# Optimization experiments

Hardware: AMD Instinct MI355X
Metric: run time of the kernel (lower is better)

## Reference

```python
import jax, jax.numpy as jnp
import numpy as np

TAU_PLUS = 0.02
TAU_MINUS = 0.02
TAU_X = 0.101
A_TRIPLET = 0.0065
HOMEOSTATIC_RATE = 0.1
DT = 0.001
SPIKE_P = 0.05  # spike probability used to binarize inputs


def setup_inputs() -> dict:
    key = jax.random.key(0)
    k1, k2, k3 = jax.random.split(key, 3)
    B, P, Q, T = 16, 2048, 2048, 256
    pre_spikes = (jax.random.uniform(k1, (B, P, T)) < SPIKE_P).astype(jnp.float32)
    post_spikes = (jax.random.uniform(k2, (B, Q, T)) < SPIKE_P).astype(jnp.float32)
    weights = jax.random.normal(k3, (P, Q), dtype=jnp.float32) * 0.1
    meta_A_plus = jnp.float32(0.01)
    meta_A_minus = jnp.float32(0.012)
    return {"pre_spikes": pre_spikes, "post_spikes": post_spikes,
            "weights": weights, "meta_A_plus": meta_A_plus,
            "meta_A_minus": meta_A_minus}


def _traces(spikes_tbn, decay):
    """Trace value used at step t: x_t = decay * (x_{t-1} + s_{t-1}), x_0 = 0."""
    def step(carry, s):
        x = decay * carry          # decayed trace, used for this step's update
        return x + s, x            # spike added AFTER the update, per original
    init = jnp.zeros(spikes_tbn.shape[1:], spikes_tbn.dtype)
    _, xs = jax.lax.scan(step, init, spikes_tbn)
    return xs  # [T, B, N]


def reference(pre_spikes, post_spikes, weights, meta_A_plus, meta_A_minus):
    B, P, T = pre_spikes.shape
    exp_plus = jnp.exp(jnp.float32(-DT / TAU_PLUS))
    exp_minus = jnp.exp(jnp.float32(-DT / TAU_MINUS))
    exp_x = jnp.exp(jnp.float32(-DT / TAU_X))

    pre_t = jnp.transpose(pre_spikes, (2, 0, 1))    # [T, B, P]
    post_t = jnp.transpose(post_spikes, (2, 0, 1))  # [T, B, Q]

    x_pre = _traces(pre_t, exp_plus)     # [T, B, P]
    x_post = _traces(post_t, exp_minus)  # [T, B, Q]
    x_trip = _traces(post_t, exp_x)      # [T, B, Q]

    # Per-step outer products summed over time == one big contraction over (t, b).
    ltp = jnp.einsum('tbp,tbq->pq', x_pre, post_t) * meta_A_plus
    triplet = jnp.einsum('tbp,tbq->pq', x_pre, post_t * x_trip) * A_TRIPLET
    ltd = jnp.einsum('tbp,tbq->pq', pre_t, x_post) * meta_A_minus
    weight_updates = ltp + triplet - ltd

    # Homeostatic scaling (fresh module: activity history holds only this sample)
    current_activity = (pre_spikes.sum() + post_spikes.sum()) / (B * T)
    scaling_factor = jnp.sqrt(HOMEOSTATIC_RATE / (current_activity + 1e-6))

    updated_weights = weights + weight_updates * scaling_factor
    return jnp.clip(updated_weights, -2.0, 2.0)
```

## Files before the change

kernel.cpp:

```cpp
#include <hip/hip_runtime.h>

constexpr int TB = 16;
constexpr int NP = 2048;
constexpr int NQ = 2048;
constexpr int TT = 256;
constexpr int KH = TB * TT;
constexpr int KT = 2 * KH;

typedef unsigned short ushort_t;
typedef __attribute__((ext_vector_type(8))) __bf16 bf16x8;
typedef __attribute__((ext_vector_type(4))) float f32x4;

__device__ __forceinline__ ushort_t f2bf(float f) {
    unsigned u = __builtin_bit_cast(unsigned, f);
    u = (u + 0x7FFFu + ((u >> 16) & 1u)) >> 16;
    return (ushort_t)u;
}

union Pack16 { ushort_t u[16]; uint4 v[2]; };

constexpr float DF1 = 0.95122942450071400910f;
constexpr float DF2 = DF1 * DF1;
constexpr float DF4 = DF2 * DF2;
constexpr float DF8 = DF4 * DF4;
constexpr float DF16 = DF8 * DF8;
constexpr float DF32 = DF16 * DF16;
constexpr float DF64 = DF32 * DF32;
constexpr float DF128 = DF64 * DF64;

constexpr float DX1 = 0.99014786386058731819f;
constexpr float DX2 = DX1 * DX1;
constexpr float DX4 = DX2 * DX2;
constexpr float DX8 = DX4 * DX4;
constexpr float DX16 = DX8 * DX8;
constexpr float DX32 = DX16 * DX16;
constexpr float DX64 = DX32 * DX32;
constexpr float DX128 = DX64 * DX64;

template <int K>
__device__ __forceinline__ float seg_step(float b, float pw, int sl) {
    float t = __shfl_up(b, K, 64);
    return (sl >= K) ? fmaf(pw, t, b) : b;
}

__global__ __launch_bounds__(256) void stage_traces(
    const float* __restrict__ pre, const float* __restrict__ post,
    const float* __restrict__ mApP, const float* __restrict__ mAmP,
    ushort_t* __restrict__ Ab, ushort_t* __restrict__ Bb,
    float* __restrict__ partials)
{
    const int tid  = threadIdx.x;
    const int lane = tid & 63;
    const int wv   = tid >> 6;
    const int sl   = lane & 15;
    const int seg  = lane >> 4;
    const int rowg = blockIdx.x * 16 + wv * 4 + seg;
    const bool isPre = rowg < TB * NP;
    const int m = isPre ? rowg : rowg - TB * NP;
    const int b = m >> 11;
    const int r = m & 2047;

    const float4* src = (const float4*)((isPre ? pre : post) + (size_t)m * TT);
    float f[16];
    #pragma unroll
    for (int j = 0; j < 4; ++j) {
        float4 u = src[sl * 4 + j];
        f[4 * j] = u.x; f[4 * j + 1] = u.y; f[4 * j + 2] = u.z; f[4 * j + 3] = u.w;
    }
    float cnt = 0.f;
    #pragma unroll
    for (int j = 0; j < 16; ++j) cnt += f[j];

    float Cf = 0.f;
    #pragma unroll
    for (int j = 0; j < 16; ++j) Cf = DF1 * (Cf + f[j]);
    float bs = Cf;
    bs = seg_step<1>(bs, DF16, sl);
    bs = seg_step<2>(bs, DF32, sl);
    bs = seg_step<4>(bs, DF64, sl);
    bs = seg_step<8>(bs, DF128, sl);
    float xinf = __shfl_up(bs, 1, 64);
    if (sl == 0) xinf = 0.f;

    float xf[16];
    {
        float x = xinf;
        #pragma unroll
        for (int j = 0; j < 16; ++j) { xf[j] = x; x = DF1 * (x + f[j]); }
    }

    Pack16 pa, pb;
    if (isPre) {
        #pragma unroll
        for (int j = 0; j < 16; ++j) {
            pa.u[j] = f2bf(xf[j]);
            pb.u[j] = (f[j] != 0.f) ? 0x3F80u : 0u;
        }
    } else {
        float Cx = 0.f;
        #pragma unroll
        for (int j = 0; j < 16; ++j) Cx = DX1 * (Cx + f[j]);
        float bx = Cx;
        bx = seg_step<1>(bx, DX16, sl);
        bx = seg_step<2>(bx, DX32, sl);
        bx = seg_step<4>(bx, DX64, sl);
        bx = seg_step<8>(bx, DX128, sl);
        float xint = __shfl_up(bx, 1, 64);
        if (sl == 0) xint = 0.f;

        const float Ap = *mApP;
        const float Am = *mAmP;
        float xt = xint;
        #pragma unroll
        for (int j = 0; j < 16; ++j) {
            pa.u[j] = (f[j] != 0.f) ? f2bf(fmaf(0.0065f, xt, Ap)) : 0u;
            pb.u[j] = f2bf(-Am * xf[j]);
            xt = DX1 * (xt + f[j]);
        }
    }

    ushort_t* o0 = (isPre ? Ab : Bb) + (size_t)r * KT + b * TT + sl * 16;
    *(uint4*)o0       = pa.v[0];
    *(uint4*)(o0 + 8) = pa.v[1];
    *(uint4*)(o0 + KH)     = pb.v[0];
    *(uint4*)(o0 + KH + 8) = pb.v[1];

    #pragma unroll
    for (int off = 32; off > 0; off >>= 1)
        cnt += __shfl_down(cnt, off, 64);
    __shared__ float wsum[4];
    if (lane == 0) wsum[wv] = cnt;
    __syncthreads();
    if (tid == 0) {
        float s = (wsum[0] + wsum[1]) + (wsum[2] + wsum[3]);
        atomicAdd(&partials[(blockIdx.x & 63) * 16], s);
    }
}

__device__ __forceinline__ void async16(const ushort_t* g, ushort_t* l) {
    __builtin_amdgcn_global_load_lds(
        (const __attribute__((address_space(1))) unsigned int*)g,
        (__attribute__((address_space(3))) unsigned int*)l,
        16, 0, 0);
}

__global__ __launch_bounds__(256) void gemm_split(
    const ushort_t* __restrict__ Ab, const ushort_t* __restrict__ Bb,
    float* __restrict__ P0, float* __restrict__ P1)
{
    __shared__ ushort_t As[2][128 * 64];
    __shared__ ushort_t Bs[2][128 * 64];

    const int tid  = threadIdx.x;
    const int lane = tid & 63;
    const int wv   = tid >> 6;
    const int wr   = wv >> 1;
    const int wc   = wv & 1;
    const int quad = lane >> 4;
    const int m16  = lane & 15;

    const int p0 = blockIdx.y * 128;
    const int q0 = blockIdx.x * 128;
    const int kbase = blockIdx.z * (KT / 2);

    const int ldsbase = wv * 64 * 8;

    f32x4 acc[4][4] = {};

    auto stage = [&](int buf, int k0) {
        #pragma unroll
        for (int rr = 0; rr < 4; ++rr) {
            const int c   = rr * 256 + tid;
            const int row = c >> 3;
            const int kk8 = (c & 7) ^ (row & 7);
            const ushort_t* ga = Ab + (size_t)(p0 + row) * KT + k0 + kk8 * 8;
            const ushort_t* gb = Bb + (size_t)(q0 + row) * KT + k0 + kk8 * 8;
            async16(ga, &As[buf][rr * 256 * 8 + ldsbase]);
            async16(gb, &Bs[buf][rr * 256 * 8 + ldsbase]);
        }
    };

    constexpr int NIT = (KT / 2) / 64;
    stage(0, kbase);

    for (int kt = 0; kt < NIT; ++kt) {
        const int cur = kt & 1;
        __syncthreads();
        if (kt + 1 < NIT)
            stage(cur ^ 1, kbase + (kt + 1) * 64);

        #pragma unroll
        for (int ks = 0; ks < 2; ++ks) {
            bf16x8 af[4], bf[4];
            #pragma unroll
            for (int i = 0; i < 4; ++i) {
                const int row  = wr * 64 + i * 16 + m16;
                const int slot = (ks * 4 + quad) ^ (row & 7);
                af[i] = *(const bf16x8*)&As[cur][row * 64 + slot * 8];
            }
            #pragma unroll
            for (int j = 0; j < 4; ++j) {
                const int row  = wc * 64 + j * 16 + m16;
                const int slot = (ks * 4 + quad) ^ (row & 7);
                bf[j] = *(const bf16x8*)&Bs[cur][row * 64 + slot * 8];
            }
            #pragma unroll
            for (int i = 0; i < 4; ++i)
                #pragma unroll
                for (int j = 0; j < 4; ++j)
                    acc[i][j] = __builtin_amdgcn_mfma_f32_16x16x32_bf16(
                        af[i], bf[j], acc[i][j], 0, 0, 0);
        }
    }

    float* P = blockIdx.z ? P1 : P0;
    #pragma unroll
    for (int i = 0; i < 4; ++i) {
        const int prow = p0 + wr * 64 + i * 16 + quad * 4;
        #pragma unroll
        for (int j = 0; j < 4; ++j) {
            const int qcol = q0 + wc * 64 + j * 16 + m16;
            #pragma unroll
            for (int r2 = 0; r2 < 4; ++r2)
                P[(size_t)(prow + r2) * NQ + qcol] = acc[i][j][r2];
        }
    }
}

__global__ __launch_bounds__(256) void merge_out(
    const float* __restrict__ W, const float* __restrict__ P1,
    const float* __restrict__ partials, float* __restrict__ Out)
{
    __shared__ float s_scale;
    const int tid = threadIdx.x;
    if (tid < 64) {
        float v = partials[tid * 16];
        #pragma unroll
        for (int off = 32; off > 0; off >>= 1)
            v += __shfl_down(v, off, 64);
        if (tid == 0)
            s_scale = sqrtf(0.1f / (v * (1.0f / 4096.0f) + 1e-6f));
    }
    __syncthreads();
    const float scale = s_scale;

    const size_t i4 = (size_t)blockIdx.x * 256 + tid;
    float4 w = ((const float4*)W)[i4];
    float4 a = ((const float4*)Out)[i4];
    float4 c = ((const float4*)P1)[i4];
    float4 o;
    o.x = fminf(fmaxf(fmaf(scale, a.x + c.x, w.x), -2.f), 2.f);
    o.y = fminf(fmaxf(fmaf(scale, a.y + c.y, w.y), -2.f), 2.f);
    o.z = fminf(fmaxf(fmaf(scale, a.z + c.z, w.z), -2.f), 2.f);
    o.w = fminf(fmaxf(fmaf(scale, a.w + c.w, w.w), -2.f), 2.f);
    ((float4*)Out)[i4] = o;
}

extern "C" void kernel_launch(void* const* d_in, const int* in_sizes, int n_in,
                              void* d_out, int out_size, void* d_ws, size_t ws_size,
                              hipStream_t stream) {
    const float* pre  = (const float*)d_in[0];
    const float* post = (const float*)d_in[1];
    const float* W    = (const float*)d_in[2];
    const float* mAp  = (const float*)d_in[3];
    const float* mAm  = (const float*)d_in[4];
    float* out = (float*)d_out;

    char* ws = (char*)d_ws;
    float* partials = (float*)ws;
    ushort_t* Ab = (ushort_t*)(ws + 16384);
    ushort_t* Bb = (ushort_t*)(ws + 16384 + (size_t)NP * KT * 2);
    float* P1    = (float*)(ws + 16384 + 2 * (size_t)NP * KT * 2);

    hipMemsetAsync(partials, 0, 64 * 16 * sizeof(float), stream);

    stage_traces<<<dim3((TB * NP + TB * NQ) / 16), dim3(256), 0, stream>>>(
        pre, post, mAp, mAm, Ab, Bb, partials);

    gemm_split<<<dim3(NQ / 128, NP / 128, 2), dim3(256), 0, stream>>>(
        Ab, Bb, out, P1);

    merge_out<<<dim3(NP * NQ / 1024), dim3(256), 0, stream>>>(
        W, P1, partials, out);
}
```

Before: 216.6 us.

## Fuse split-K merge and epilogue into GEMM via per-tile arrival counters

Removes the separate merge kernel. Each of the two split-K blocks for a tile writes its partial and then bumps an atomic counter, and the second block to arrive adds the other partial, applies the homeostatic scale, adds W and clamps. The K loop is also manually unrolled by two with precomputed, incrementing global pointers, and launch bounds request two blocks per CU. This saves a kernel launch and one full re-read of the output, but still writes both partials and relies on threadfence ordering between blocks.

Result: slower. 325.8 us (+50.4%).

```diff
diff --git a/kernel.cpp b/kernel.cpp
--- a/kernel.cpp
+++ b/kernel.cpp
@@ -144,9 +144,11 @@
         16, 0, 0);
 }
 
-__global__ __launch_bounds__(256) void gemm_split(
+__global__ __launch_bounds__(256, 2) void gemm_fused(
     const ushort_t* __restrict__ Ab, const ushort_t* __restrict__ Bb,
-    float* __restrict__ P0, float* __restrict__ P1)
+    const float* __restrict__ W, const float* __restrict__ partials,
+    int* __restrict__ flags, float* __restrict__ P0, float* __restrict__ P1,
+    float* __restrict__ Out)
 {
     __shared__ ushort_t As[2][128 * 64];
     __shared__ ushort_t Bs[2][128 * 64];
@@ -162,33 +164,31 @@
     const int p0 = blockIdx.y * 128;
     const int q0 = blockIdx.x * 128;
     const int kbase = blockIdx.z * (KT / 2);
-
-    const int ldsbase = wv * 64 * 8;
+    const int ldsbase = wv * 512;
+
+    const ushort_t* gaP[4];
+    const ushort_t* gbP[4];
+    #pragma unroll
+    for (int rr = 0; rr < 4; ++rr) {
+        const int c   = rr * 256 + tid;
+        const int row = c >> 3;
+        const int kk8 = (c & 7) ^ (row & 7);
+        gaP[rr] = Ab + (size_t)(p0 + row) * KT + kbase + kk8 * 8;
+        gbP[rr] = Bb + (size_t)(q0 + row) * KT + kbase + kk8 * 8;
+    }
 
     f32x4 acc[4][4] = {};
 
-    auto stage = [&](int buf, int k0) {
+    auto stageF = [&](int buf) {
         #pragma unroll
         for (int rr = 0; rr < 4; ++rr) {
-            const int c   = rr * 256 + tid;
-            const int row = c >> 3;
-            const int kk8 = (c & 7) ^ (row & 7);
-            const ushort_t* ga = Ab + (size_t)(p0 + row) * KT + k0 + kk8 * 8;
-            const ushort_t* gb = Bb + (size_t)(q0 + row) * KT + k0 + kk8 * 8;
-            async16(ga, &As[buf][rr * 256 * 8 + ldsbase]);
-            async16(gb, &Bs[buf][rr * 256 * 8 + ldsbase]);
+            async16(gaP[rr], &As[buf][rr * 2048 + ldsbase]);
+            async16(gbP[rr], &Bs[buf][rr * 2048 + ldsbase]);
+            gaP[rr] += 64;
+            gbP[rr] += 64;
         }
     };
-
-    constexpr int NIT = (KT / 2) / 64;
-    stage(0, kbase);
-
-    for (int kt = 0; kt < NIT; ++kt) {
-        const int cur = kt & 1;
-        __syncthreads();
-        if (kt + 1 < NIT)
-            stage(cur ^ 1, kbase + (kt + 1) * 64);
-
+    auto computeF = [&](int buf) {
         #pragma unroll
         for (int ks = 0; ks < 2; ++ks) {
             bf16x8 af[4], bf[4];
@@ -196,13 +196,13 @@
             for (int i = 0; i < 4; ++i) {
                 const int row  = wr * 64 + i * 16 + m16;
                 const int slot = (ks * 4 + quad) ^ (row & 7);
-                af[i] = *(const bf16x8*)&As[cur][row * 64 + slot * 8];
+                af[i] = *(const bf16x8*)&As[buf][row * 64 + slot * 8];
             }
             #pragma unroll
             for (int j = 0; j < 4; ++j) {
                 const int row  = wc * 64 + j * 16 + m16;
                 const int slot = (ks * 4 + quad) ^ (row & 7);
-                bf[j] = *(const bf16x8*)&Bs[cur][row * 64 + slot * 8];
+                bf[j] = *(const bf16x8*)&Bs[buf][row * 64 + slot * 8];
             }
             #pragma unroll
             for (int i = 0; i < 4; ++i)
@@ -211,9 +211,21 @@
                     acc[i][j] = __builtin_amdgcn_mfma_f32_16x16x32_bf16(
                         af[i], bf[j], acc[i][j], 0, 0, 0);
         }
-    }
-
-    float* P = blockIdx.z ? P1 : P0;
+    };
+
+    constexpr int NIT = (KT / 2) / 64;
+    stageF(0);
+    for (int kt2 = 0; kt2 < NIT / 2; ++kt2) {
+        __syncthreads();
+        stageF(1);
+        computeF(0);
+        __syncthreads();
+        if (kt2 + 1 < NIT / 2)
+            stageF(0);
+        computeF(1);
+    }
+
+    float* Pmine = blockIdx.z ? P1 : P0;
     #pragma unroll
     for (int i = 0; i < 4; ++i) {
         const int prow = p0 + wr * 64 + i * 16 + quad * 4;
@@ -222,38 +234,42 @@
             const int qcol = q0 + wc * 64 + j * 16 + m16;
             #pragma unroll
             for (int r2 = 0; r2 < 4; ++r2)
-                P[(size_t)(prow + r2) * NQ + qcol] = acc[i][j][r2];
-        }
-    }
-}
-
-__global__ __launch_bounds__(256) void merge_out(
-    const float* __restrict__ W, const float* __restrict__ P1,
-    const float* __restrict__ partials, float* __restrict__ Out)
-{
-    __shared__ float s_scale;
-    const int tid = threadIdx.x;
-    if (tid < 64) {
-        float v = partials[tid * 16];
-        #pragma unroll
-        for (int off = 32; off > 0; off >>= 1)
-            v += __shfl_down(v, off, 64);
-        if (tid == 0)
-            s_scale = sqrtf(0.1f / (v * (1.0f / 4096.0f) + 1e-6f));
-    }
+                Pmine[(size_t)(prow + r2) * NQ + qcol] = acc[i][j][r2];
+        }
+    }
+
+    __threadfence();
     __syncthreads();
-    const float scale = s_scale;
-
-    const size_t i4 = (size_t)blockIdx.x * 256 + tid;
-    float4 w = ((const float4*)W)[i4];
-    float4 a = ((const float4*)Out)[i4];
-    float4 c = ((const float4*)P1)[i4];
-    float4 o;
-    o.x = fminf(fmaxf(fmaf(scale, a.x + c.x, w.x), -2.f), 2.f);
-    o.y = fminf(fmaxf(fmaf(scale, a.y + c.y, w.y), -2.f), 2.f);
-    o.z = fminf(fmaxf(fmaf(scale, a.z + c.z, w.z), -2.f), 2.f);
-    o.w = fminf(fmaxf(fmaf(scale, a.w + c.w, w.w), -2.f), 2.f);
-    ((float4*)Out)[i4] = o;
+    __shared__ int s_old;
+    if (tid == 0)
+        s_old = atomicAdd(&flags[blockIdx.y * 16 + blockIdx.x], 1);
+    __syncthreads();
+    if (s_old != 1) return;
+
+    __threadfence();
+    const float* Pother = blockIdx.z ? P0 : P1;
+
+    float v = partials[lane * 16];
+    #pragma unroll
+    for (int off = 32; off > 0; off >>= 1)
+        v += __shfl_xor(v, off, 64);
+    const float scale = sqrtf(0.1f / (v * (1.0f / 4096.0f) + 1e-6f));
+
+    #pragma unroll
+    for (int i = 0; i < 4; ++i) {
+        const int prow = p0 + wr * 64 + i * 16 + quad * 4;
+        #pragma unroll
+        for (int j = 0; j < 4; ++j) {
+            const int qcol = q0 + wc * 64 + j * 16 + m16;
+            #pragma unroll
+            for (int r2 = 0; r2 < 4; ++r2) {
+                const size_t idx = (size_t)(prow + r2) * NQ + qcol;
+                float o = fmaf(scale, acc[i][j][r2] + Pother[idx], W[idx]);
+                o = fminf(fmaxf(o, -2.f), 2.f);
+                Out[idx] = o;
+            }
+        }
+    }
 }
 
 extern "C" void kernel_launch(void* const* d_in, const int* in_sizes, int n_in,
@@ -268,18 +284,16 @@
 
     char* ws = (char*)d_ws;
     float* partials = (float*)ws;
-    ushort_t* Ab = (ushort_t*)(ws + 16384);
-    ushort_t* Bb = (ushort_t*)(ws + 16384 + (size_t)NP * KT * 2);
-    float* P1    = (float*)(ws + 16384 + 2 * (size_t)NP * KT * 2);
-
-    hipMemsetAsync(partials, 0, 64 * 16 * sizeof(float), stream);
+    int* flags      = (int*)(ws + 16384);
+    ushort_t* Ab = (ushort_t*)(ws + 32768);
+    ushort_t* Bb = (ushort_t*)(ws + 32768 + (size_t)NP * KT * 2);
+    float* P1    = (float*)(ws + 32768 + 2 * (size_t)NP * KT * 2);
+
+    hipMemsetAsync(ws, 0, 32768, stream);
 
     stage_traces<<<dim3((TB * NP + TB * NQ) / 16), dim3(256), 0, stream>>>(
         pre, post, mAp, mAm, Ab, Bb, partials);
 
-    gemm_split<<<dim3(NQ / 128, NP / 128, 2), dim3(256), 0, stream>>>(
-        Ab, Bb, out, P1);
-
-    merge_out<<<dim3(NP * NQ / 1024), dim3(256), 0, stream>>>(
-        W, P1, partials, out);
-}
+    gemm_fused<<<dim3(NQ / 128, NP / 128, 2), dim3(256), 0, stream>>>(
+        Ab, Bb, W, partials, flags, out, P1, out);
+}
```
